# Kernel optimization log

Measured on AMD Instinct MI355X. Metric: run time of the kernel, lower is better.

Reference implementation:

```python
import jax, jax.numpy as jnp
import numpy as np

B, S, H, HID, V, NSPEC = 8, 4096, 1024, 128, 60000, 5
EPS = 1e-12
SLOPE = 0.01  # nn.LeakyReLU default negative_slope


def _leaky(x):
    return jnp.where(x >= 0, x, SLOPE * x)


def setup_inputs() -> dict:
    key = jax.random.key(0)
    ks = jax.random.split(key, 12)
    gene_ids = jax.random.randint(ks[0], (B, S), 0, V)
    cont = jax.random.uniform(ks[1], (B, S), jnp.float32, 0.0, 10.0)
    spec_mask = jax.random.uniform(ks[2], (B, S)) < 0.05
    spec_vals = -jax.random.randint(ks[3], (B, S), 1, NSPEC + 1).astype(jnp.float32)
    expr_values = jnp.where(spec_mask, spec_vals, cont)
    gene_emb = jax.random.normal(ks[4], (V, H), jnp.float32) * 0.02
    W1 = jax.random.normal(ks[5], (HID,), jnp.float32) * 0.5   # Linear(1,128) weight
    b1 = jax.random.normal(ks[6], (HID,), jnp.float32) * 0.1
    W2 = jax.random.normal(ks[7], (HID, H), jnp.float32) * 0.05  # Linear(128,H)
    b2 = jax.random.normal(ks[8], (H,), jnp.float32) * 0.1
    special_emb = jax.random.normal(ks[9], (NSPEC, HID), jnp.float32) * 0.02
    special_emb = special_emb.at[2].set(0.0)  # padding_idx=2
    pos_emb = jax.random.normal(ks[10], (S, H), jnp.float32) * 0.02
    gamma = jnp.ones((H,), jnp.float32)
    beta = jnp.zeros((H,), jnp.float32)
    return dict(gene_ids=gene_ids, expr_values=expr_values, gene_emb=gene_emb,
                W1=W1, b1=b1, W2=W2, b2=b2, special_emb=special_emb,
                pos_emb=pos_emb, gamma=gamma, beta=beta)


def reference(gene_ids, expr_values, gene_emb, W1, b1, W2, b2, special_emb,
              pos_emb, gamma, beta):
    x = expr_values                                  # [B,S]
    special = x < 0                                  # special-token mask
    # mapped special id: -(int(x)+1); clamp so gather is in-range on non-special slots
    mapped = jnp.clip(-(x.astype(jnp.int32) + 1), 0, NSPEC - 1)
    spec_e = special_emb[mapped]                     # [B,S,HID] gather
    cont_e = _leaky(x[..., None] * W1 + b1)          # dense_1 on scalar value
    h = jnp.where(special[..., None], spec_e, cont_e)  # scatter-combine
    expr_e = _leaky(h) @ W2 + b2                     # dense_2 -> [B,S,H]
    emb = gene_emb[gene_ids] + expr_e + pos_emb[None, :, :]
    mu = jnp.mean(emb, axis=-1, keepdims=True)
    var = jnp.mean(jnp.square(emb - mu), axis=-1, keepdims=True)
    out = (emb - mu) * jax.lax.rsqrt(var + EPS) * gamma + beta
    return out  # dropout is identity at inference (p used at train only)
```

## Files before the change

kernel.cpp:

```cpp
#include <hip/hip_runtime.h>
#include <hip/hip_bf16.h>

#define B_DIM   8
#define S_LEN   4096
#define H_DIM   1024
#define HID_DIM 128
#define NSPEC   5
#define NROWS   (HID_DIM + 1 + NSPEC)
#define SLOPE   0.01f
#define LN_EPS  1e-12f

typedef float vfloat4 __attribute__((ext_vector_type(4)));

__global__ __launch_bounds__(256) void build_kernel(
        const float* __restrict__ W1,
        const float* __restrict__ b1,
        const float* __restrict__ W2,
        const float* __restrict__ b2,
        const float* __restrict__ spec,
        float* __restrict__ tvals,
        float2* __restrict__ tab) {
    const int row = blockIdx.x;
    const int tid = threadIdx.x;

    __shared__ float tsh[HID_DIM];
    __shared__ float ash[HID_DIM];
    __shared__ float csh[HID_DIM];

    float w = 0.0f, b = 0.0f, t = 0.0f;
    if (tid < HID_DIM) {
        w = W1[tid];
        b = b1[tid];
        t = (w != 0.0f) ? (-b / w) : __builtin_inff();
        tsh[tid] = t;
        if (row == 0) tvals[tid] = t;
    }
    __syncthreads();
    if (tid < HID_DIM) {
        int r = 0;
        #pragma unroll 8
        for (int k2 = 0; k2 < HID_DIM; ++k2) {
            const float t2 = tsh[k2];
            if (t2 < t || (t2 == t && k2 < tid)) ++r;
        }

        float a, c;
        if (row <= HID_DIM) {
            const bool crossed = (r < row);
            bool zpos;
            if (w > 0.0f)      zpos = crossed;
            else if (w < 0.0f) zpos = !crossed;
            else               zpos = (b >= 0.0f);
            const float s = zpos ? 1.0f : (SLOPE * SLOPE);
            a = s * w;
            c = s * b;
        } else {
            const int m = row - (HID_DIM + 1);
            const float e = spec[m * HID_DIM + tid];
            a = 0.0f;
            c = (e >= 0.0f) ? e : SLOPE * e;
        }
        ash[tid] = a;
        csh[tid] = c;
    }
    __syncthreads();

    float4 u = make_float4(0.f, 0.f, 0.f, 0.f);
    float4 v = make_float4(0.f, 0.f, 0.f, 0.f);
    #pragma unroll 4
    for (int k = 0; k < HID_DIM; ++k) {
        const float4 w2 = reinterpret_cast<const float4*>(W2 + (size_t)k * H_DIM)[tid];
        const float a = ash[k], c = csh[k];
        u.x = fmaf(a, w2.x, u.x);  v.x = fmaf(c, w2.x, v.x);
        u.y = fmaf(a, w2.y, u.y);  v.y = fmaf(c, w2.y, v.y);
        u.z = fmaf(a, w2.z, u.z);  v.z = fmaf(c, w2.z, v.z);
        u.w = fmaf(a, w2.w, u.w);  v.w = fmaf(c, w2.w, v.w);
    }
    const float4 bb = reinterpret_cast<const float4*>(b2)[tid];
    float4* trow = reinterpret_cast<float4*>(tab + (size_t)row * H_DIM);
    trow[2 * tid]     = make_float4(u.x, v.x + bb.x, u.y, v.y + bb.y);
    trow[2 * tid + 1] = make_float4(u.z, v.z + bb.z, u.w, v.w + bb.w);
}

__global__ __launch_bounds__(256, 4) void fuse_kernel(
        const int*   __restrict__ gene_ids,
        const float* __restrict__ expr,
        const float* __restrict__ gene_emb,
        const float* __restrict__ pos_emb,
        const float* __restrict__ gamma,
        const float* __restrict__ beta,
        const float* __restrict__ tvals,
        const float2* __restrict__ tab,
        float* __restrict__ out) {
    const int tid  = threadIdx.x;
    const int lane = tid & 63;
    const int t    = blockIdx.x * 4 + (tid >> 6);
    const int sp   = t & (S_LEN - 1);

    const float x   = expr[t];
    const int   gid = gene_ids[t];
    const float tka = tvals[lane];
    const float tkb = tvals[lane + 64];

    const float4* gp = reinterpret_cast<const float4*>(gene_emb + (size_t)gid * H_DIM);
    const float4* pp = reinterpret_cast<const float4*>(pos_emb  + (size_t)sp  * H_DIM);

    float4 g[4], p[4];
    #pragma unroll
    for (int q = 0; q < 4; ++q) {
        const int f = lane + 64 * q;
        g[q] = gp[f];
        p[q] = pp[f];
    }

    const int rc = __popcll(__ballot(tka <= x)) + __popcll(__ballot(tkb <= x));
    const bool spec = (x < 0.0f);
    const int  msp  = min(max(-((int)x) - 1, 0), NSPEC - 1);
    const int  row  = spec ? (HID_DIM + 1 + msp) : rc;
    const float xm  = spec ? 0.0f : x;

    const float4* tp = reinterpret_cast<const float4*>(tab + (size_t)row * H_DIM);
    float4 ta[4], tb[4];
    #pragma unroll
    for (int q = 0; q < 4; ++q) {
        const int f = lane + 64 * q;
        ta[q] = tp[2 * f];
        tb[q] = tp[2 * f + 1];
    }

    float4 e[4];
    float s1 = 0.0f, s2 = 0.0f;
    #pragma unroll
    for (int q = 0; q < 4; ++q) {
        float4 ev;
        ev.x = g[q].x + fmaf(xm, ta[q].x, ta[q].y) + p[q].x;
        ev.y = g[q].y + fmaf(xm, ta[q].z, ta[q].w) + p[q].y;
        ev.z = g[q].z + fmaf(xm, tb[q].x, tb[q].y) + p[q].z;
        ev.w = g[q].w + fmaf(xm, tb[q].z, tb[q].w) + p[q].w;
        e[q] = ev;
        s1 += ev.x + ev.y + ev.z + ev.w;
        s2 += ev.x * ev.x + ev.y * ev.y + ev.z * ev.z + ev.w * ev.w;
    }

    float4 gm[4], bt[4];
    #pragma unroll
    for (int q = 0; q < 4; ++q) {
        const int f = lane + 64 * q;
        gm[q] = reinterpret_cast<const float4*>(gamma)[f];
        bt[q] = reinterpret_cast<const float4*>(beta)[f];
    }

    #pragma unroll
    for (int off = 32; off >= 1; off >>= 1) {
        s1 += __shfl_xor(s1, off, 64);
        s2 += __shfl_xor(s2, off, 64);
    }

    const float inv  = 1.0f / (float)H_DIM;
    const float mu   = s1 * inv;
    const float rsig = rsqrtf(s2 * inv - mu * mu + LN_EPS);

    vfloat4* op = reinterpret_cast<vfloat4*>(out + (size_t)t * H_DIM);
    #pragma unroll
    for (int q = 0; q < 4; ++q) {
        const int f = lane + 64 * q;
        vfloat4 o;
        o.x = fmaf((e[q].x - mu) * rsig, gm[q].x, bt[q].x);
        o.y = fmaf((e[q].y - mu) * rsig, gm[q].y, bt[q].y);
        o.z = fmaf((e[q].z - mu) * rsig, gm[q].z, bt[q].z);
        o.w = fmaf((e[q].w - mu) * rsig, gm[q].w, bt[q].w);
        __builtin_nontemporal_store(o, op + f);
    }
}

extern "C" void kernel_launch(void* const* d_in, const int* in_sizes, int n_in,
                              void* d_out, int out_size, void* d_ws, size_t ws_size,
                              hipStream_t stream) {
    const int*   gene_ids = (const int*)  d_in[0];
    const float* expr     = (const float*)d_in[1];
    const float* gene_emb = (const float*)d_in[2];
    const float* W1       = (const float*)d_in[3];
    const float* b1       = (const float*)d_in[4];
    const float* W2       = (const float*)d_in[5];
    const float* b2       = (const float*)d_in[6];
    const float* spec     = (const float*)d_in[7];
    const float* pos_emb  = (const float*)d_in[8];
    const float* gamma    = (const float*)d_in[9];
    const float* beta     = (const float*)d_in[10];
    float* out = (float*)d_out;

    const size_t tab_bytes = (size_t)NROWS * H_DIM * sizeof(float2);
    float2* tab   = (float2*)d_ws;
    float*  tvals = (float*)((char*)d_ws + tab_bytes);

    const int n_tokens = in_sizes[0];

    build_kernel<<<NROWS, 256, 0, stream>>>(W1, b1, W2, b2, spec, tvals, tab);
    fuse_kernel<<<n_tokens / 4, 256, 0, stream>>>(gene_ids, expr, gene_emb, pos_emb,
                                                  gamma, beta, tvals, tab, out);
}
```

Before: 73.95 us.

## Make fuse kernel persistent grid-stride, reusing pos_emb rows and staging gamma/beta

The fuse kernel now launches a fixed grid of 2048 blocks that loop over token groups. Its token stride is a multiple of the sequence length, so each wave loads its pos_emb row once and reuses it on every iteration. Gamma and beta are staged once per block in LDS, and the next token's expr value and gene id are prefetched one iteration ahead. The goal is less redundant memory traffic and lower per-block setup cost. In exchange, each wave's loads are serialized across iterations and fewer independent waves are in flight.

```diff
diff --git a/kernel.cpp b/kernel.cpp
--- a/kernel.cpp
+++ b/kernel.cpp
@@ -9,6 +9,7 @@
 #define NROWS   (HID_DIM + 1 + NSPEC)
 #define SLOPE   0.01f
 #define LN_EPS  1e-12f
+#define FUSE_GRID 2048
 
 typedef float vfloat4 __attribute__((ext_vector_type(4)));
 
@@ -91,85 +92,103 @@
         const float* __restrict__ beta,
         const float* __restrict__ tvals,
         const float2* __restrict__ tab,
-        float* __restrict__ out) {
+        float* __restrict__ out,
+        int ngroups) {
     const int tid  = threadIdx.x;
     const int lane = tid & 63;
-    const int t    = blockIdx.x * 4 + (tid >> 6);
-    const int sp   = t & (S_LEN - 1);
-
-    const float x   = expr[t];
-    const int   gid = gene_ids[t];
+    const int wv   = tid >> 6;
+
+    __shared__ float4 gm_lds[H_DIM / 4];
+    __shared__ float4 bt_lds[H_DIM / 4];
+    gm_lds[tid] = reinterpret_cast<const float4*>(gamma)[tid];
+    bt_lds[tid] = reinterpret_cast<const float4*>(beta)[tid];
+
     const float tka = tvals[lane];
     const float tkb = tvals[lane + 64];
 
-    const float4* gp = reinterpret_cast<const float4*>(gene_emb + (size_t)gid * H_DIM);
-    const float4* pp = reinterpret_cast<const float4*>(pos_emb  + (size_t)sp  * H_DIM);
-
-    float4 g[4], p[4];
+    const int t_first = blockIdx.x * 4 + wv;
+    const int sp      = t_first & (S_LEN - 1);
+    const float4* pp  = reinterpret_cast<const float4*>(pos_emb + (size_t)sp * H_DIM);
+    float4 p[4];
     #pragma unroll
-    for (int q = 0; q < 4; ++q) {
-        const int f = lane + 64 * q;
-        g[q] = gp[f];
-        p[q] = pp[f];
-    }
-
-    const int rc = __popcll(__ballot(tka <= x)) + __popcll(__ballot(tkb <= x));
-    const bool spec = (x < 0.0f);
-    const int  msp  = min(max(-((int)x) - 1, 0), NSPEC - 1);
-    const int  row  = spec ? (HID_DIM + 1 + msp) : rc;
-    const float xm  = spec ? 0.0f : x;
-
-    const float4* tp = reinterpret_cast<const float4*>(tab + (size_t)row * H_DIM);
-    float4 ta[4], tb[4];
-    #pragma unroll
-    for (int q = 0; q < 4; ++q) {
-        const int f = lane + 64 * q;
-        ta[q] = tp[2 * f];
-        tb[q] = tp[2 * f + 1];
-    }
-
-    float4 e[4];
-    float s1 = 0.0f, s2 = 0.0f;
-    #pragma unroll
-    for (int q = 0; q < 4; ++q) {
-        float4 ev;
-        ev.x = g[q].x + fmaf(xm, ta[q].x, ta[q].y) + p[q].x;
-        ev.y = g[q].y + fmaf(xm, ta[q].z, ta[q].w) + p[q].y;
-        ev.z = g[q].z + fmaf(xm, tb[q].x, tb[q].y) + p[q].z;
-        ev.w = g[q].w + fmaf(xm, tb[q].z, tb[q].w) + p[q].w;
-        e[q] = ev;
-        s1 += ev.x + ev.y + ev.z + ev.w;
-        s2 += ev.x * ev.x + ev.y * ev.y + ev.z * ev.z + ev.w * ev.w;
-    }
-
-    float4 gm[4], bt[4];
-    #pragma unroll
-    for (int q = 0; q < 4; ++q) {
-        const int f = lane + 64 * q;
-        gm[q] = reinterpret_cast<const float4*>(gamma)[f];
-        bt[q] = reinterpret_cast<const float4*>(beta)[f];
-    }
-
-    #pragma unroll
-    for (int off = 32; off >= 1; off >>= 1) {
-        s1 += __shfl_xor(s1, off, 64);
-        s2 += __shfl_xor(s2, off, 64);
-    }
-
-    const float inv  = 1.0f / (float)H_DIM;
-    const float mu   = s1 * inv;
-    const float rsig = rsqrtf(s2 * inv - mu * mu + LN_EPS);
-
-    vfloat4* op = reinterpret_cast<vfloat4*>(out + (size_t)t * H_DIM);
-    #pragma unroll
-    for (int q = 0; q < 4; ++q) {
-        const int f = lane + 64 * q;
-        vfloat4 o;
-        o.x = fmaf((e[q].x - mu) * rsig, gm[q].x, bt[q].x);
-        o.y = fmaf((e[q].y - mu) * rsig, gm[q].y, bt[q].y);
-        o.z = fmaf((e[q].z - mu) * rsig, gm[q].z, bt[q].z);
-        o.w = fmaf((e[q].w - mu) * rsig, gm[q].w, bt[q].w);
-        __builtin_nontemporal_store(o, op + f);
+    for (int q = 0; q < 4; ++q) p[q] = pp[lane + 64 * q];
+
+    __syncthreads();
+
+    float x   = expr[t_first];
+    int   gid = gene_ids[t_first];
+
+    for (int grp = blockIdx.x; grp < ngroups; grp += gridDim.x) {
+        const int t = grp * 4 + wv;
+
+        const int tn = t + 4 * gridDim.x;
+        float nx  = 0.0f;
+        int   ngid = 0;
+        if (tn < 4 * ngroups) {
+            nx   = expr[tn];
+            ngid = gene_ids[tn];
+        }
+
+        const float4* gp = reinterpret_cast<const float4*>(gene_emb + (size_t)gid * H_DIM);
+        float4 g[4];
+        #pragma unroll
+        for (int q = 0; q < 4; ++q) g[q] = gp[lane + 64 * q];
+
+        const int rc = __popcll(__ballot(tka <= x)) + __popcll(__ballot(tkb <= x));
+        const bool spc = (x < 0.0f);
+        const int  msp = min(max(-((int)x) - 1, 0), NSPEC - 1);
+        const int  row = spc ? (HID_DIM + 1 + msp) : rc;
+        const float xm = spc ? 0.0f : x;
+
+        const float4* tp = reinterpret_cast<const float4*>(tab + (size_t)row * H_DIM);
+        float4 ta[4], tb[4];
+        #pragma unroll
+        for (int q = 0; q < 4; ++q) {
+            const int f = lane + 64 * q;
+            ta[q] = tp[2 * f];
+            tb[q] = tp[2 * f + 1];
+        }
+
+        float4 e[4];
+        float s1 = 0.0f, s2 = 0.0f;
+        #pragma unroll
+        for (int q = 0; q < 4; ++q) {
+            float4 ev;
+            ev.x = g[q].x + fmaf(xm, ta[q].x, ta[q].y) + p[q].x;
+            ev.y = g[q].y + fmaf(xm, ta[q].z, ta[q].w) + p[q].y;
+            ev.z = g[q].z + fmaf(xm, tb[q].x, tb[q].y) + p[q].z;
+            ev.w = g[q].w + fmaf(xm, tb[q].z, tb[q].w) + p[q].w;
+            e[q] = ev;
+            s1 += ev.x + ev.y + ev.z + ev.w;
+            s2 += ev.x * ev.x + ev.y * ev.y + ev.z * ev.z + ev.w * ev.w;
+        }
+
+        #pragma unroll
+        for (int off = 32; off >= 1; off >>= 1) {
+            s1 += __shfl_xor(s1, off, 64);
+            s2 += __shfl_xor(s2, off, 64);
+        }
+
+        const float inv  = 1.0f / (float)H_DIM;
+        const float mu   = s1 * inv;
+        const float rsig = rsqrtf(s2 * inv - mu * mu + LN_EPS);
+
+        vfloat4* op = reinterpret_cast<vfloat4*>(out + (size_t)t * H_DIM);
+        #pragma unroll
+        for (int q = 0; q < 4; ++q) {
+            const int f = lane + 64 * q;
+            const float4 gm = gm_lds[f];
+            const float4 bt = bt_lds[f];
+            vfloat4 o;
+            o.x = fmaf((e[q].x - mu) * rsig, gm.x, bt.x);
+            o.y = fmaf((e[q].y - mu) * rsig, gm.y, bt.y);
+            o.z = fmaf((e[q].z - mu) * rsig, gm.z, bt.z);
+            o.w = fmaf((e[q].w - mu) * rsig, gm.w, bt.w);
+            __builtin_nontemporal_store(o, op + f);
+        }
+
+        x   = nx;
+        gid = ngid;
     }
 }
 
@@ -194,8 +213,9 @@
     float*  tvals = (float*)((char*)d_ws + tab_bytes);
 
     const int n_tokens = in_sizes[0];
+    const int ngroups  = n_tokens / 4;
 
     build_kernel<<<NROWS, 256, 0, stream>>>(W1, b1, W2, b2, spec, tvals, tab);
-    fuse_kernel<<<n_tokens / 4, 256, 0, stream>>>(gene_ids, expr, gene_emb, pos_emb,
-                                                  gamma, beta, tvals, tab, out);
+    fuse_kernel<<<FUSE_GRID, 256, 0, stream>>>(gene_ids, expr, gene_emb, pos_emb,
+                                               gamma, beta, tvals, tab, out, ngroups);
 }
```

After: 67.89 us. 1.09x faster.
